# Performance work log

Measured on AMD Instinct MI355X. Metric: run time of the kernel, lower is better.

The kernel has to match this reference:

```python
import jax, jax.numpy as jnp
import numpy as np

B, T, HID = 2, 2048, 2048
NH, NKV = 16, 8
NOPE, ROPE = 128, 64
HD = NOPE + ROPE  # 192
VD = 128
KV_RANK, Q_RANK = 512, 1536
EPS = 1e-6
THETA = 10000.0
GROUPS = NH // NKV


def rmsnorm(x, w):
    var = jnp.mean(x * x, axis=-1, keepdims=True)
    return x * jax.lax.rsqrt(var + EPS) * w


def rope_cos_sin(seq_len, dtype):
    inv_freq = 1.0 / (THETA ** (jnp.arange(0, ROPE, 2, dtype=jnp.float32) / ROPE))
    t = jnp.arange(seq_len, dtype=jnp.float32)
    freqs = jnp.outer(t, inv_freq)
    emb = jnp.concatenate([freqs, freqs], axis=-1)  # [T, ROPE]
    return jnp.cos(emb).astype(dtype)[None, :, None, :], jnp.sin(emb).astype(dtype)[None, :, None, :]


def rotate_half(x):
    x1, x2 = x[..., : x.shape[-1] // 2], x[..., x.shape[-1] // 2 :]
    return jnp.concatenate([-x2, x1], axis=-1)


def setup_inputs() -> dict:
    key = jax.random.key(0)
    ks = jax.random.split(key, 7)
    s = 0.02
    return {
        "hidden_states": jax.random.normal(ks[0], (B, T, HID), jnp.float32),
        "q_a_w": jax.random.normal(ks[1], (HID, Q_RANK), jnp.float32) * s,
        "q_a_ln_w": jnp.ones((Q_RANK,), jnp.float32),
        "q_b_w": jax.random.normal(ks[2], (Q_RANK, NH * HD), jnp.float32) * s,
        "kv_a_w": jax.random.normal(ks[3], (HID, KV_RANK + NKV * ROPE), jnp.float32) * s,
        "kv_a_ln_w": jnp.ones((KV_RANK,), jnp.float32),
        "kv_b_w": jax.random.normal(ks[4], (KV_RANK, NKV * (NOPE + VD)), jnp.float32) * s,
        "o_w": jax.random.normal(ks[5], (NH * VD, HID), jnp.float32) * s,
    }


def reference(hidden_states, q_a_w, q_a_ln_w, q_b_w, kv_a_w, kv_a_ln_w, kv_b_w, o_w):
    x = hidden_states
    # Q low-rank path: a_proj -> RMSNorm -> b_proj
    q = rmsnorm(x @ q_a_w, q_a_ln_w) @ q_b_w
    q = q.reshape(B, T, NH, HD)
    q_nope, q_rope = q[..., :NOPE], q[..., NOPE:]
    # KV low-rank + decoupled rope key
    kv_raw = x @ kv_a_w
    kv_latent = rmsnorm(kv_raw[..., :KV_RANK], kv_a_ln_w)
    k_rope = kv_raw[..., KV_RANK:].reshape(B, T, NKV, ROPE)
    kv = (kv_latent @ kv_b_w).reshape(B, T, NKV, NOPE + VD)
    k_nope, v = kv[..., :NOPE], kv[..., NOPE:]
    # partial RoPE on rope slice only
    cos, sin = rope_cos_sin(T, x.dtype)
    q_rope = q_rope * cos + rotate_half(q_rope) * sin
    k_rope = k_rope * cos + rotate_half(k_rope) * sin
    q_full = jnp.concatenate([q_nope, q_rope], axis=-1)  # [B,T,NH,HD]
    k_full = jnp.concatenate([k_nope, k_rope], axis=-1)  # [B,T,NKV,HD]
    # GQA expansion (repeat_interleave over head dim)
    k_full = jnp.repeat(k_full, GROUPS, axis=2)  # [B,T,NH,HD]
    v_full = jnp.repeat(v, GROUPS, axis=2)       # [B,T,NH,VD]
    scale = HD ** -0.5
    scores = jnp.einsum("bqhd,bkhd->bhqk", q_full, k_full) * scale
    probs = jax.nn.softmax(scores, axis=-1)
    attn = jnp.einsum("bhqk,bkhd->bqhd", probs, v_full)
    out = attn.reshape(B, T, NH * VD) @ o_w
    return out
```

## Files before the change

kernel.cpp:

```cpp
#include <hip/hip_runtime.h>

using u16 = unsigned short;
using u32 = unsigned int;

typedef float f32x4 __attribute__((ext_vector_type(4)));
typedef __bf16 bf16x8 __attribute__((ext_vector_type(8)));

__device__ __forceinline__ u16 f2bf(float f){
  u32 u = __builtin_bit_cast(u32, f);
  u32 r = (u + 0x7fffu + ((u >> 16) & 1u)) >> 16;
  return (u16)r;
}
__device__ __forceinline__ float bf2f(u16 h){
  u32 u = ((u32)h) << 16;
  return __builtin_bit_cast(float, u);
}
__device__ __forceinline__ void gl2lds16(const void* g, void* l){
  __builtin_amdgcn_global_load_lds((const __attribute__((address_space(1))) u32*)g,
                                   (__attribute__((address_space(3))) u32*)l, 16, 0, 0);
}
__device__ __forceinline__ int swz24(int ck, int r){ return (ck & 24) | ((ck ^ r) & 7); }
__device__ __forceinline__ u32 cvtpk_bf16(float a, float b){
  u32 r; asm("v_cvt_pk_bf16_f32 %0, %1, %2" : "=v"(r) : "v"(a), "v"(b)); return r;
}
__device__ __forceinline__ float exp2_raw(float x){
  float r; asm("v_exp_f32 %0, %1" : "=v"(r) : "v"(x)); return r;
}

__global__ __launch_bounds__(256) void prep_kernel(const float* __restrict__ hs, u16* __restrict__ XB,
                                                   const float* __restrict__ q_a_w,  u16* __restrict__ Wqa,
                                                   const float* __restrict__ kv_a_w, u16* __restrict__ Wkva,
                                                   const float* __restrict__ q_b_w,  u16* __restrict__ Wqb,
                                                   const float* __restrict__ kv_b_w, u16* __restrict__ Wkvb,
                                                   const float* __restrict__ o_w,    u16* __restrict__ Wo,
                                                   float* __restrict__ cosT, float* __restrict__ sinT){
  __shared__ float tile[32][33];
  const int id = blockIdx.x;
  if (id >= 15104){
    long i = ((long)(id - 15104)*256 + threadIdx.x)*4;
    float4 v = *(const float4*)(hs + i);
    u16 o[4] = { f2bf(v.x), f2bf(v.y), f2bf(v.z), f2bf(v.w) };
    *(ushort4*)(XB + i) = *(ushort4*)o;
    return;
  }
  if (id >= 14848){
    int idx = (id - 14848)*256 + threadIdx.x;
    int t = idx >> 5, d = idx & 31;
    double inv = pow(10000.0, -(double)d / 32.0);
    double a = (double)t * inv;
    cosT[idx] = (float)cos(a);
    sinT[idx] = (float)sin(a);
    return;
  }
  const float* in; u16* out; int K, N, lid;
  if      (id <  3072){ in = q_a_w;  out = Wqa;  K = 2048; N = 1536; lid = id; }
  else if (id <  5120){ in = kv_a_w; out = Wkva; K = 2048; N = 1024; lid = id - 3072; }
  else if (id <  9728){ in = q_b_w;  out = Wqb;  K = 1536; N = 3072; lid = id - 5120; }
  else if (id < 10752){ in = kv_b_w; out = Wkvb; K =  512; N = 2048; lid = id - 9728; }
  else                { in = o_w;    out = Wo;   K = 2048; N = 2048; lid = id - 10752; }
  const int tx = threadIdx.x & 31, ty = threadIdx.x >> 5;
  const int nb = N >> 5;
  const int n0 = (lid % nb)*32, k0 = (lid / nb)*32;
  for (int i = ty; i < 32; i += 8)
    tile[i][tx] = in[(size_t)(k0+i)*N + n0+tx];
  __syncthreads();
  for (int i = ty; i < 32; i += 8)
    out[(size_t)(n0+i)*K + k0+tx] = f2bf(tile[tx][i]);
}

__device__ __forceinline__ void remap_id(int id, int& bx, int& by){
  bx = id >> 5;
  by = ((id & 7) << 2) | ((id >> 3) & 3);
}

template<int OUT_BF16>
__global__ __launch_bounds__(256) void gemm_bt(const u16* __restrict__ A,
                                               const u16* __restrict__ Bt,
                                               void* __restrict__ Cout,
                                               int M, int N, int K, float cscale){
  __shared__ u16 As[128*32];
  __shared__ u16 Bs[128*32];
  const int tid = threadIdx.x, lane = tid & 63, wave = tid >> 6;
  int bx, by; remap_id(blockIdx.y*gridDim.x + blockIdx.x, bx, by);
  const int m0 = by*128, n0 = bx*128;
  const int wm = (wave >> 1)*64, wn = (wave & 1)*64;
  const int g = lane >> 4, lr = lane & 15;
  f32x4 acc[4][4] = {};
  const int sr = (wave*2)*16 + (lane >> 2);
  const int sc = (lane & 3)*8;
  for (int k0 = 0; k0 < K; k0 += 32){
    __syncthreads();
    #pragma unroll
    for (int i = 0; i < 2; i++){
      int c = wave*2 + i;
      int r = sr + i*16;
      gl2lds16(A  + (size_t)(m0+r)*K + k0 + sc, (char*)As + c*1024);
      gl2lds16(Bt + (size_t)(n0+r)*K + k0 + sc, (char*)Bs + c*1024);
    }
    __syncthreads();
    bf16x8 af[4], bfr[4];
    #pragma unroll
    for (int mi = 0; mi < 4; mi++) af[mi]  = *reinterpret_cast<const bf16x8*>(&As[(wm+mi*16+lr)*32 + g*8]);
    #pragma unroll
    for (int ni = 0; ni < 4; ni++) bfr[ni] = *reinterpret_cast<const bf16x8*>(&Bs[(wn+ni*16+lr)*32 + g*8]);
    #pragma unroll
    for (int mi = 0; mi < 4; mi++)
      #pragma unroll
      for (int ni = 0; ni < 4; ni++)
        acc[mi][ni] = __builtin_amdgcn_mfma_f32_16x16x32_bf16(af[mi], bfr[ni], acc[mi][ni], 0,0,0);
  }
  #pragma unroll
  for (int mi = 0; mi < 4; mi++)
    #pragma unroll
    for (int ni = 0; ni < 4; ni++)
      #pragma unroll
      for (int r = 0; r < 4; r++){
        int row = m0 + wm + mi*16 + g*4 + r;
        int col = n0 + wn + ni*16 + lr;
        float v = acc[mi][ni][r];
        if (OUT_BF16) ((u16*)Cout)[(size_t)row*N + col] = f2bf(v*cscale);
        else          ((float*)Cout)[(size_t)row*N + col] = v;
      }
}

__global__ __launch_bounds__(256) void gemm_qb_kvb(const u16* __restrict__ Qlat,
                                                   const u16* __restrict__ Wqb,
                                                   u16* __restrict__ QB,
                                                   const float* __restrict__ cosT,
                                                   const float* __restrict__ sinT,
                                                   const u16* __restrict__ KVlat,
                                                   const u16* __restrict__ Wkvb,
                                                   u16* __restrict__ KVB){
  constexpr float qscale = 0.07216878364870322f * 1.44269504088896340f;
  __shared__ u16 As[128*32];
  __shared__ u16 Bs[128*32];
  const int id = blockIdx.x;
  const u16 *A, *Bt; u16* C; int N, K; bool isqb;
  int bx, by;
  if (id < 768){ A = Qlat;  Bt = Wqb;  C = QB;  N = 3072; K = 1536; isqb = true;  remap_id(id, bx, by); }
  else         { A = KVlat; Bt = Wkvb; C = KVB; N = 2048; K =  512; isqb = false; remap_id(id - 768, bx, by); }
  const int tid = threadIdx.x, lane = tid & 63, wave = tid >> 6;
  const int m0 = by*128, n0 = bx*128;
  const int wm = (wave >> 1)*64, wn = (wave & 1)*64;
  const int g = lane >> 4, lr = lane & 15;
  f32x4 acc[4][4] = {};
  const int sr = (wave*2)*16 + (lane >> 2);
  const int sc = (lane & 3)*8;
  for (int k0 = 0; k0 < K; k0 += 32){
    __syncthreads();
    #pragma unroll
    for (int i = 0; i < 2; i++){
      int c = wave*2 + i;
      int r = sr + i*16;
      gl2lds16(A  + (size_t)(m0+r)*K + k0 + sc, (char*)As + c*1024);
      gl2lds16(Bt + (size_t)(n0+r)*K + k0 + sc, (char*)Bs + c*1024);
    }
    __syncthreads();
    bf16x8 af[4], bfr[4];
    #pragma unroll
    for (int mi = 0; mi < 4; mi++) af[mi]  = *reinterpret_cast<const bf16x8*>(&As[(wm+mi*16+lr)*32 + g*8]);
    #pragma unroll
    for (int ni = 0; ni < 4; ni++) bfr[ni] = *reinterpret_cast<const bf16x8*>(&Bs[(wn+ni*16+lr)*32 + g*8]);
    #pragma unroll
    for (int mi = 0; mi < 4; mi++)
      #pragma unroll
      for (int ni = 0; ni < 4; ni++)
        acc[mi][ni] = __builtin_amdgcn_mfma_f32_16x16x32_bf16(af[mi], bfr[ni], acc[mi][ni], 0,0,0);
  }
  if (isqb){
    const bool rope = (((n0 + wn) >> 6) % 3) == 2;
    #pragma unroll
    for (int mi = 0; mi < 4; mi++)
      #pragma unroll
      for (int r = 0; r < 4; r++){
        int row = m0 + wm + mi*16 + g*4 + r;
        int t = row & 2047;
        u16* crow = C + (size_t)row*3072 + n0 + wn;
        if (rope){
          #pragma unroll
          for (int np = 0; np < 2; np++){
            int dp = np*16 + lr;
            float x1 = acc[mi][np][r]*qscale, x2 = acc[mi][np+2][r]*qscale;
            float cv = cosT[t*32 + dp], sv = sinT[t*32 + dp];
            crow[dp]      = f2bf(x1*cv - x2*sv);
            crow[dp + 32] = f2bf(x2*cv + x1*sv);
          }
        } else {
          #pragma unroll
          for (int ni = 0; ni < 4; ni++)
            crow[ni*16 + lr] = f2bf(acc[mi][ni][r]*qscale);
        }
      }
  } else {
    #pragma unroll
    for (int mi = 0; mi < 4; mi++)
      #pragma unroll
      for (int ni = 0; ni < 4; ni++)
        #pragma unroll
        for (int r = 0; r < 4; r++){
          int row = m0 + wm + mi*16 + g*4 + r;
          int col = n0 + wn + ni*16 + lr;
          C[(size_t)row*2048 + col] = f2bf(acc[mi][ni][r]);
        }
  }
}

__global__ __launch_bounds__(256) void norm_split(const u16* __restrict__ R23,
                                                  const float* __restrict__ q_ln,
                                                  const float* __restrict__ kv_ln,
                                                  const float* __restrict__ cosT,
                                                  const float* __restrict__ sinT,
                                                  u16* __restrict__ Qlat,
                                                  u16* __restrict__ KVlat,
                                                  u16* __restrict__ Kf){
  int row = blockIdx.x;
  int t = row & 2047, b = row >> 11;
  const u16* x = R23 + (size_t)row*2560;
  int c = threadIdx.x;
  float xq[8]; float ssq = 0.f;
  if (c < 192){
    ushort4 a = *(const ushort4*)(x + c*8);
    ushort4 bq = *(const ushort4*)(x + c*8 + 4);
    u16 e[8] = {a.x,a.y,a.z,a.w,bq.x,bq.y,bq.z,bq.w};
    #pragma unroll
    for (int j = 0; j < 8; j++){ xq[j] = bf2f(e[j]); ssq += xq[j]*xq[j]; }
  }
  float xk[4]; float ssk = 0.f;
  if (c < 128){
    ushort4 a = *(const ushort4*)(x + 1536 + c*4);
    u16 e[4] = {a.x,a.y,a.z,a.w};
    #pragma unroll
    for (int j = 0; j < 4; j++){ xk[j] = bf2f(e[j]); ssk += xk[j]*xk[j]; }
  }
  #pragma unroll
  for (int m = 1; m < 64; m <<= 1){
    ssq += __shfl_xor(ssq, m, 64);
    ssk += __shfl_xor(ssk, m, 64);
  }
  __shared__ float pq[4], pk[4];
  if ((c & 63) == 0){ pq[c >> 6] = ssq; pk[c >> 6] = ssk; }
  __syncthreads();
  float invq = rsqrtf((pq[0]+pq[1]+pq[2]+pq[3]) / 1536.0f + 1e-6f);
  float invk = rsqrtf((pk[0]+pk[1]+pk[2]+pk[3]) / 512.0f + 1e-6f);
  if (c < 192){
    u16 o[8];
    #pragma unroll
    for (int j = 0; j < 8; j++) o[j] = f2bf(xq[j]*invq*q_ln[c*8+j]);
    *(ushort4*)(Qlat + (size_t)row*1536 + c*8)     = *(ushort4*)o;
    *(ushort4*)(Qlat + (size_t)row*1536 + c*8 + 4) = *(ushort4*)(o+4);
  }
  if (c < 128){
    u16 o[4];
    #pragma unroll
    for (int j = 0; j < 4; j++) o[j] = f2bf(xk[j]*invk*kv_ln[c*4+j]);
    *(ushort4*)(KVlat + (size_t)row*512 + c*4) = *(ushort4*)o;
  }
  int kh = c >> 5, dp = c & 31;
  float x1 = bf2f(x[2048 + kh*64 + dp]), x2 = bf2f(x[2048 + kh*64 + dp + 32]);
  float cv = cosT[t*32 + dp], sv = sinT[t*32 + dp];
  float o1 = x1*cv - x2*sv;
  float o2 = x2*cv + x1*sv;
  u16* kr = Kf + ((size_t)(b*8 + kh)*2048 + t)*192;
  int c1 = 128 + dp, c2 = 128 + dp + 32;
  kr[(swz24(c1 >> 3, t) << 3) | (c1 & 7)] = f2bf(o1);
  kr[(swz24(c2 >> 3, t) << 3) | (c2 & 7)] = f2bf(o2);
}

__global__ __launch_bounds__(256) void kv_rearrange(const u16* __restrict__ kv,
                                                    u16* __restrict__ vT,
                                                    u16* __restrict__ Kf){
  int bid = blockIdx.x;
  int tt = bid & 31, kvh = (bid >> 5) & 7, b = bid >> 8;
  int t0 = tt*64;
  __shared__ u16 tile[64][136];
  int tid = threadIdx.x;
  #pragma unroll
  for (int i = 0; i < 4; i++){
    int c2 = tid + i*256;
    int rr = c2 >> 4, ck = c2 & 15;
    int t = t0 + rr;
    int ck2 = (ck & 8) | ((ck ^ t) & 7);
    uint4 v = *(const uint4*)(kv + ((size_t)(b*2048 + t))*2048 + kvh*256 + ck*8);
    *(uint4*)(Kf + ((size_t)(b*8 + kvh)*2048 + t)*192 + ck2*8) = v;
  }
  #pragma unroll
  for (int i = 0; i < 4; i++){
    int c = tid + i*256;
    int r = c >> 4, ck = c & 15;
    const u16* src = kv + ((size_t)(b*2048 + t0 + r))*2048 + kvh*256 + 128 + ck*8;
    *(uint4*)&tile[r][ck*8] = *(const uint4*)src;
  }
  __syncthreads();
  #pragma unroll
  for (int i = 0; i < 4; i++){
    int c = tid + i*256;
    int vd = c >> 3, tc = c & 7;
    int stc = tc ^ (vd & 7);
    uint4 tv;
    u16* tp = (u16*)&tv;
    #pragma unroll
    for (int j = 0; j < 8; j++) tp[j] = tile[tc*8 + j][vd];
    *(uint4*)(vT + ((size_t)(b*8 + kvh)*128 + vd)*2048 + t0 + stc*8) = tv;
  }
}

__global__ __launch_bounds__(256, 2) void attn_kernel(const u16* __restrict__ Q,
                                                      const u16* __restrict__ Kf,
                                                      const u16* __restrict__ Vt,
                                                      u16* __restrict__ Oa){
  constexpr int T = 2048;
  constexpr int NT = T/64;
  __shared__ u16 Ks[64*192];
  __shared__ u16 Vs[2][128*64];
  __shared__ u16 Ps[4][2048];
  const int tid = threadIdx.x, lane = tid & 63, wave = tid >> 6;
  const int g = lane >> 4, lr = lane & 15;

  const int wg = blockIdx.x;
  const int role = (wg & 7)*64 + (wg >> 3);
  const int grp = role >> 5;
  const int b = grp >> 3, kvh = grp & 7;
  const int within = role & 31;
  const int h = kvh*2 + (within >> 4);
  const int q0 = (within & 15)*128 + wave*32;

  bf16x8 aq[2][6];
  #pragma unroll
  for (int qg = 0; qg < 2; qg++){
    const u16* qrow = Q + ((size_t)b*T + q0 + qg*16 + lr)*3072 + h*192;
    #pragma unroll
    for (int kc = 0; kc < 6; kc++)
      aq[qg][kc] = *reinterpret_cast<const bf16x8*>(qrow + kc*32 + g*8);
  }
  const u16* Kbase = Kf + (size_t)(b*8 + kvh)*T*192;
  const u16* Vbase = Vt + (size_t)(b*8 + kvh)*128*T;

  f32x4 ovb[2][8] = {};
  float mq[2] = {-1e30f, -1e30f};
  float lq[2] = {0.f, 0.f};

  auto stageK = [&](int kt){
    const u16* ksrc = Kbase + (size_t)kt*12288 + wave*3072 + lane*8;
    #pragma unroll
    for (int i = 0; i < 6; i++)
      gl2lds16(ksrc + i*512, (char*)Ks + (wave*6 + i)*1024);
  };
  auto stageV = [&](int kt, int buf){
    #pragma unroll
    for (int i = 0; i < 4; i++){
      int c = wave*4 + i;
      const u16* vsrc = Vbase + (size_t)(c*8 + (lane >> 3))*T + kt*64 + (lane & 7)*8;
      gl2lds16(vsrc, (char*)(&Vs[0][0]) + buf*16384 + c*1024);
    }
  };

  stageK(0);
  stageV(0, 0);
  __syncthreads();

  int buf = 0;
  for (int kt = 0; kt < NT; kt++){
    const bool notlast = (kt + 1 < NT);
    if (notlast) stageV(kt + 1, buf ^ 1);

    f32x4 s[2][4];
    __builtin_amdgcn_s_setprio(1);
    #pragma unroll
    for (int nb = 0; nb < 4; nb++){
      const int row = nb*16 + lr;
      f32x4 a0 = {0.f,0.f,0.f,0.f}, a1 = {0.f,0.f,0.f,0.f};
      #pragma unroll
      for (int kc = 0; kc < 6; kc++){
        int ckl = swz24(kc*4 + g, row);
        bf16x8 kf = *reinterpret_cast<const bf16x8*>(&Ks[row*192 + ckl*8]);
        a0 = __builtin_amdgcn_mfma_f32_16x16x32_bf16(kf, aq[0][kc], a0, 0,0,0);
        a1 = __builtin_amdgcn_mfma_f32_16x16x32_bf16(kf, aq[1][kc], a1, 0,0,0);
      }
      s[0][nb] = a0; s[1][nb] = a1;
    }
    __builtin_amdgcn_s_setprio(0);

    asm volatile("s_waitcnt lgkmcnt(0)" ::: "memory");
    __builtin_amdgcn_s_barrier();
    __builtin_amdgcn_sched_barrier(0);
    if (notlast) stageK(kt + 1);

    #pragma unroll
    for (int qg = 0; qg < 2; qg++){
      float pm = s[qg][0][0];
      #pragma unroll
      for (int nb = 0; nb < 4; nb++)
        #pragma unroll
        for (int r = 0; r < 4; r++)
          if (nb || r) pm = fmaxf(pm, s[qg][nb][r]);
      pm = fmaxf(pm, __shfl_xor(pm, 16, 64));
      pm = fmaxf(pm, __shfl_xor(pm, 32, 64));
      if (!__all(pm <= mq[qg] + 8.f)){
        float mn = fmaxf(mq[qg], pm);
        float corr = exp2_raw(mq[qg] - mn);
        mq[qg] = mn;
        lq[qg] *= corr;
        #pragma unroll
        for (int r = 0; r < 4; r++){
          float cr = __shfl(corr, (lane & 48) | (g*4 + r), 64);
          #pragma unroll
          for (int vb = 0; vb < 8; vb++) ovb[qg][vb][r] *= cr;
        }
      }
      float ls = 0.f;
      #pragma unroll
      for (int nb = 0; nb < 4; nb++){
        float e0 = exp2_raw(s[qg][nb][0] - mq[qg]);
        float e1 = exp2_raw(s[qg][nb][1] - mq[qg]);
        float e2 = exp2_raw(s[qg][nb][2] - mq[qg]);
        float e3 = exp2_raw(s[qg][nb][3] - mq[qg]);
        ls += (e0 + e1) + (e2 + e3);
        int stc = (2*nb + (g >> 1)) ^ (lr & 7);
        volatile u32* p = (volatile u32*)&Ps[wave][qg*1024 + lr*64 + stc*8 + (g & 1)*4];
        p[0] = cvtpk_bf16(e0, e1);
        p[1] = cvtpk_bf16(e2, e3);
      }
      lq[qg] += ls;
    }


    bf16x8 ap[2][2];
    #pragma unroll
    for (int qg = 0; qg < 2; qg++)
      #pragma unroll
      for (int k2 = 0; k2 < 2; k2++){
        int ck = (k2*4 + g) ^ (lr & 7);
        ap[qg][k2] = *reinterpret_cast<const bf16x8*>(&Ps[wave][qg*1024 + lr*64 + ck*8]);
      }
    __builtin_amdgcn_s_setprio(1);
    #pragma unroll
    for (int vb = 0; vb < 8; vb++)
      #pragma unroll
      for (int k2 = 0; k2 < 2; k2++){
        int vd = vb*16 + lr;
        int ck = (k2*4 + g) ^ (vd & 7);
        bf16x8 bv = *reinterpret_cast<const bf16x8*>(&Vs[buf][vd*64 + ck*8]);
        ovb[0][vb] = __builtin_amdgcn_mfma_f32_16x16x32_bf16(ap[0][k2], bv, ovb[0][vb], 0,0,0);
        ovb[1][vb] = __builtin_amdgcn_mfma_f32_16x16x32_bf16(ap[1][k2], bv, ovb[1][vb], 0,0,0);
      }
    __builtin_amdgcn_s_setprio(0);

    if (notlast) __syncthreads();
    buf ^= 1;
  }

  #pragma unroll
  for (int qg = 0; qg < 2; qg++){
    float lt = lq[qg];
    lt += __shfl_xor(lt, 16, 64);
    lt += __shfl_xor(lt, 32, 64);
    float invq = 1.0f / lt;
    float inv_r[4];
    #pragma unroll
    for (int r = 0; r < 4; r++)
      inv_r[r] = __shfl(invq, (lane & 48) | (g*4 + r), 64);
    u16* obase = Oa + ((size_t)b*T + q0 + qg*16)*2048 + h*128;
    #pragma unroll
    for (int vb = 0; vb < 8; vb++)
      #pragma unroll
      for (int r = 0; r < 4; r++)
        obase[(size_t)(g*4 + r)*2048 + vb*16 + lr] = f2bf(ovb[qg][vb][r]*inv_r[r]);
  }
}

extern "C" void kernel_launch(void* const* d_in, const int* in_sizes, int n_in,
                              void* d_out, int out_size, void* d_ws, size_t ws_size,
                              hipStream_t stream){
  const float* hs      = (const float*)d_in[0];
  const float* q_a_w   = (const float*)d_in[1];
  const float* q_a_ln  = (const float*)d_in[2];
  const float* q_b_w   = (const float*)d_in[3];
  const float* kv_a_w  = (const float*)d_in[4];
  const float* kv_a_ln = (const float*)d_in[5];
  const float* kv_b_w  = (const float*)d_in[6];
  const float* o_w     = (const float*)d_in[7];

  char* ws = (char*)d_ws;
  size_t off = 0;
  auto alloc = [&](size_t bytes){ void* p = ws + off; off += bytes; return p; };
  u16*  Wqa   = (u16*)alloc(1536ull*2048*2);
  u16*  Wkva  = (u16*)alloc(1024ull*2048*2);
  u16*  Wqb   = (u16*)alloc(3072ull*1536*2);
  u16*  Wkvb  = (u16*)alloc(2048ull*512*2);
  u16*  Wo    = (u16*)alloc(2048ull*2048*2);
  u16*  XB    = (u16*)alloc(4096ull*2048*2);
  u16*  R23   = (u16*)alloc(4096ull*2560*2);
  u16*  QB    = (u16*)alloc(4096ull*3072*2);
  u16*  Qlat  = (u16*)alloc(4096ull*1536*2);
  u16*  KVlat = (u16*)alloc(4096ull*512*2);
  u16*  Kf    = (u16*)alloc(2ull*8*2048*192*2);
  u16*  Vt    = (u16*)alloc(2ull*8*128*2048*2);
  float* cosT = (float*)alloc(2048ull*32*4);
  float* sinT = (float*)alloc(2048ull*32*4);
  (void)ws_size; (void)in_sizes; (void)n_in; (void)out_size;

  u16* KVB = R23;

  prep_kernel<<<23296, 256, 0, stream>>>(hs, XB, q_a_w, Wqa, kv_a_w, Wkva,
                                         q_b_w, Wqb, kv_b_w, Wkvb, o_w, Wo, cosT, sinT);
  gemm_bt<1><<<dim3(20, 32), 256, 0, stream>>>(XB, Wqa, R23, 4096, 2560, 2048, 1.0f);
  norm_split<<<4096, 256, 0, stream>>>(R23, q_a_ln, kv_a_ln, cosT, sinT, Qlat, KVlat, Kf);
  gemm_qb_kvb<<<1280, 256, 0, stream>>>(Qlat, Wqb, QB, cosT, sinT, KVlat, Wkvb, KVB);
  kv_rearrange<<<512, 256, 0, stream>>>(KVB, Vt, Kf);
  attn_kernel<<<512, 256, 0, stream>>>(QB, Kf, Vt, XB);
  gemm_bt<0><<<dim3(16, 32), 256, 0, stream>>>(XB, Wo, (float*)d_out, 4096, 2048, 2048, 1.0f);
}
```

Baseline: 347.0 us.

## Single-buffer V and halve P scratch to fit three blocks per CU

Result: slower. 522.3 us (+50.5%).

```diff
diff --git a/kernel.cpp b/kernel.cpp
--- a/kernel.cpp
+++ b/kernel.cpp
@@ -304,15 +304,15 @@
   }
 }
 
-__global__ __launch_bounds__(256, 2) void attn_kernel(const u16* __restrict__ Q,
+__global__ __launch_bounds__(256, 3) void attn_kernel(const u16* __restrict__ Q,
                                                       const u16* __restrict__ Kf,
                                                       const u16* __restrict__ Vt,
                                                       u16* __restrict__ Oa){
   constexpr int T = 2048;
   constexpr int NT = T/64;
   __shared__ u16 Ks[64*192];
-  __shared__ u16 Vs[2][128*64];
-  __shared__ u16 Ps[4][2048];
+  __shared__ u16 Vs[128*64];
+  __shared__ u16 Ps[4][1024];
   const int tid = threadIdx.x, lane = tid & 63, wave = tid >> 6;
   const int g = lane >> 4, lr = lane & 15;
 
@@ -345,23 +345,21 @@
     for (int i = 0; i < 6; i++)
       gl2lds16(ksrc + i*512, (char*)Ks + (wave*6 + i)*1024);
   };
-  auto stageV = [&](int kt, int buf){
+  auto stageV = [&](int kt){
     #pragma unroll
     for (int i = 0; i < 4; i++){
       int c = wave*4 + i;
       const u16* vsrc = Vbase + (size_t)(c*8 + (lane >> 3))*T + kt*64 + (lane & 7)*8;
-      gl2lds16(vsrc, (char*)(&Vs[0][0]) + buf*16384 + c*1024);
+      gl2lds16(vsrc, (char*)Vs + c*1024);
     }
   };
 
   stageK(0);
-  stageV(0, 0);
+  stageV(0);
   __syncthreads();
 
-  int buf = 0;
   for (int kt = 0; kt < NT; kt++){
     const bool notlast = (kt + 1 < NT);
-    if (notlast) stageV(kt + 1, buf ^ 1);
 
     f32x4 s[2][4];
     __builtin_amdgcn_s_setprio(1);
@@ -380,9 +378,7 @@
     }
     __builtin_amdgcn_s_setprio(0);
 
-    asm volatile("s_waitcnt lgkmcnt(0)" ::: "memory");
-    __builtin_amdgcn_s_barrier();
-    __builtin_amdgcn_sched_barrier(0);
+    __syncthreads();
     if (notlast) stageK(kt + 1);
 
     #pragma unroll
@@ -416,37 +412,35 @@
         float e3 = exp2_raw(s[qg][nb][3] - mq[qg]);
         ls += (e0 + e1) + (e2 + e3);
         int stc = (2*nb + (g >> 1)) ^ (lr & 7);
-        volatile u32* p = (volatile u32*)&Ps[wave][qg*1024 + lr*64 + stc*8 + (g & 1)*4];
+        volatile u32* p = (volatile u32*)&Ps[wave][lr*64 + stc*8 + (g & 1)*4];
         p[0] = cvtpk_bf16(e0, e1);
         p[1] = cvtpk_bf16(e2, e3);
       }
       lq[qg] += ls;
-    }
-
-
-    bf16x8 ap[2][2];
-    #pragma unroll
-    for (int qg = 0; qg < 2; qg++)
+
+      bf16x8 ap[2];
       #pragma unroll
       for (int k2 = 0; k2 < 2; k2++){
         int ck = (k2*4 + g) ^ (lr & 7);
-        ap[qg][k2] = *reinterpret_cast<const bf16x8*>(&Ps[wave][qg*1024 + lr*64 + ck*8]);
+        ap[k2] = *reinterpret_cast<const bf16x8*>(&Ps[wave][lr*64 + ck*8]);
       }
-    __builtin_amdgcn_s_setprio(1);
-    #pragma unroll
-    for (int vb = 0; vb < 8; vb++)
-      #pragma unroll
-      for (int k2 = 0; k2 < 2; k2++){
-        int vd = vb*16 + lr;
-        int ck = (k2*4 + g) ^ (vd & 7);
-        bf16x8 bv = *reinterpret_cast<const bf16x8*>(&Vs[buf][vd*64 + ck*8]);
-        ovb[0][vb] = __builtin_amdgcn_mfma_f32_16x16x32_bf16(ap[0][k2], bv, ovb[0][vb], 0,0,0);
-        ovb[1][vb] = __builtin_amdgcn_mfma_f32_16x16x32_bf16(ap[1][k2], bv, ovb[1][vb], 0,0,0);
-      }
-    __builtin_amdgcn_s_setprio(0);
-
-    if (notlast) __syncthreads();
-    buf ^= 1;
+      __builtin_amdgcn_s_setprio(1);
+      #pragma unroll
+      for (int vb = 0; vb < 8; vb++)
+        #pragma unroll
+        for (int k2 = 0; k2 < 2; k2++){
+          int vd = vb*16 + lr;
+          int ck = (k2*4 + g) ^ (vd & 7);
+          bf16x8 bv = *reinterpret_cast<const bf16x8*>(&Vs[vd*64 + ck*8]);
+          ovb[qg][vb] = __builtin_amdgcn_mfma_f32_16x16x32_bf16(ap[k2], bv, ovb[qg][vb], 0,0,0);
+        }
+      __builtin_amdgcn_s_setprio(0);
+    }
+
+    if (notlast){
+      __syncthreads();
+      stageV(kt + 1);
+    }
   }
 
   #pragma unroll
```
